# Performance work log

Hardware: AMD Instinct MI355X
Metric: run time of the kernel (lower is better)

## Reference

```python
import jax, jax.numpy as jnp
import numpy as np

N, E, D, H = 40000, 640000, 128, 8
DH = D // H  # out_feats per head
EPS = 1e-5


def _layernorm(x, g, b):
    mu = jnp.mean(x, axis=-1, keepdims=True)
    var = jnp.mean(jnp.square(x - mu), axis=-1, keepdims=True)
    return (x - mu) * jax.lax.rsqrt(var + EPS) * g + b


def setup_inputs() -> dict:
    key = jax.random.key(0)
    ks = jax.random.split(key, 12)
    s = 0.02
    return {
        "feat": jax.random.normal(ks[0], (N, D), dtype=jnp.float32),
        "src": jax.random.randint(ks[1], (E,), 0, N, dtype=jnp.int32),
        "dst": jax.random.randint(ks[2], (E,), 0, N, dtype=jnp.int32),
        "Wq": jax.random.normal(ks[3], (D, D), dtype=jnp.float32) * s,
        "Wk": jax.random.normal(ks[4], (D, D), dtype=jnp.float32) * s,
        "Wv": jax.random.normal(ks[5], (D, D), dtype=jnp.float32) * s,
        "ln1_g": jnp.ones((D,), jnp.float32),
        "ln1_b": jnp.zeros((D,), jnp.float32),
        "ln2_g": jnp.ones((D,), jnp.float32),
        "ln2_b": jnp.zeros((D,), jnp.float32),
        "W1": jax.random.normal(ks[6], (D, 4 * D), dtype=jnp.float32) * s,
        "b1": jnp.zeros((4 * D,), jnp.float32),
        "prelu_w": jnp.full((4 * D,), 0.25, jnp.float32),
        "W2": jax.random.normal(ks[7], (4 * D, D), dtype=jnp.float32) * s,
        "b2": jnp.zeros((D,), jnp.float32),
    }


def reference(feat, src, dst, Wq, Wk, Wv, ln1_g, ln1_b, ln2_g, ln2_b,
              W1, b1, prelu_w, W2, b2):
    n = feat.shape[0]
    feat_c = jax.lax.stop_gradient(feat)  # .clone().detach()
    q = (feat @ Wq).reshape(n, H, DH)
    k = (feat_c @ Wk).reshape(n, H, DH)
    v = (feat_c @ Wv).reshape(n, H, DH)

    # u_dot_v: per-edge, per-head dot product of k at src and q at dst
    scores = jnp.einsum('ehd,ehd->eh', k[src], q[dst]) / np.float32(np.sqrt(DH * H))

    # edge_softmax: softmax over incoming edges of each destination node
    smax = jax.ops.segment_max(scores, dst, num_segments=n)  # [N,H]
    sexp = jnp.exp(scores - smax[dst])
    ssum = jax.ops.segment_sum(sexp, dst, num_segments=n)
    a = sexp / ssum[dst]  # [E,H]  (attn_drop is eval no-op)

    # u_mul_e + sum: weighted scatter-aggregate of v[src] into dst
    msgs = v[src] * a[:, :, None]  # [E,H,DH]
    ft2 = jax.ops.segment_sum(msgs, dst, num_segments=n).reshape(n, D)

    rst = _layernorm(ft2 + feat, ln1_g, ln1_b)
    h = rst @ W1 + b1
    h = jnp.where(h >= 0, h, prelu_w * h)  # PReLU, per-channel
    ffn = h @ W2 + b2  # ffn_drop is eval no-op
    return _layernorm(rst + ffn, ln2_g, ln2_b)
```

## Files before the change

kernel.cpp:

```cpp
#include <hip/hip_runtime.h>
#include <hip/hip_bf16.h>
#include <math.h>

#define DIM 128
#define NHEAD 8
#define DHEAD 16
#define HID 512
#define LN_EPS 1e-5f
#define QSCALE 0.12751879104863297f

typedef __bf16 bf16x8 __attribute__((ext_vector_type(8)));
typedef float f32x4 __attribute__((ext_vector_type(4)));
typedef float f32x2 __attribute__((ext_vector_type(2)));
typedef _Float16 f16x2 __attribute__((ext_vector_type(2)));

__device__ inline float bf2f(unsigned int bits16) {
    return __uint_as_float(bits16 << 16);
}
__device__ inline unsigned short f2bf(float f) {
    unsigned int u = __float_as_uint(f);
    unsigned int r = u + 0x7fff + ((u >> 16) & 1);
    return (unsigned short)(r >> 16);
}
__device__ inline unsigned short f2h(float f) {
    _Float16 h = (_Float16)f;
    return __builtin_bit_cast(unsigned short, h);
}
__device__ inline float h2f(unsigned short h) {
    return (float)__builtin_bit_cast(_Float16, h);
}
__device__ inline unsigned short pk_fp8(float a, float b) {
    int r = __builtin_amdgcn_cvt_pk_fp8_f32(a, b, 0, false);
    return (unsigned short)(r & 0xffff);
}
__device__ inline f32x2 unpk_fp8_lo(unsigned int w) {
    return __builtin_amdgcn_cvt_pk_f32_fp8((int)w, false);
}
__device__ inline f32x2 unpk_fp8_hi(unsigned int w) {
    return __builtin_amdgcn_cvt_pk_f32_fp8((int)w, true);
}
__device__ inline float fexp2(float x) { return __builtin_amdgcn_exp2f(x); }

__device__ inline void gload_lds16(const void* g, void* l) {
    __builtin_amdgcn_global_load_lds(
        (const __attribute__((address_space(1))) unsigned int*)g,
        (__attribute__((address_space(3))) unsigned int*)l, 16, 0, 0);
}

__device__ __forceinline__ float dot16_fp8(uint4 w, const float (&q)[16]) {
    f32x2 a0 = unpk_fp8_lo(w.x), b0 = unpk_fp8_hi(w.x);
    f32x2 a1 = unpk_fp8_lo(w.y), b1 = unpk_fp8_hi(w.y);
    f32x2 a2 = unpk_fp8_lo(w.z), b2 = unpk_fp8_hi(w.z);
    f32x2 a3 = unpk_fp8_lo(w.w), b3 = unpk_fp8_hi(w.w);
    float t0 = fmaf(a0.x, q[0],  fmaf(a0.y, q[1],  fmaf(b0.x, q[2],  b0.y * q[3])));
    float t1 = fmaf(a1.x, q[4],  fmaf(a1.y, q[5],  fmaf(b1.x, q[6],  b1.y * q[7])));
    float t2 = fmaf(a2.x, q[8],  fmaf(a2.y, q[9],  fmaf(b2.x, q[10], b2.y * q[11])));
    float t3 = fmaf(a3.x, q[12], fmaf(a3.y, q[13], fmaf(b3.x, q[14], b3.y * q[15])));
    return (t0 + t1) + (t2 + t3);
}

__device__ __forceinline__ void pv16_fp8(uint4 w, float wt, float (&acc)[16]) {
    f32x2 a0 = unpk_fp8_lo(w.x), b0 = unpk_fp8_hi(w.x);
    f32x2 a1 = unpk_fp8_lo(w.y), b1 = unpk_fp8_hi(w.y);
    f32x2 a2 = unpk_fp8_lo(w.z), b2 = unpk_fp8_hi(w.z);
    f32x2 a3 = unpk_fp8_lo(w.w), b3 = unpk_fp8_hi(w.w);
    acc[0]  = fmaf(a0.x, wt, acc[0]);  acc[1]  = fmaf(a0.y, wt, acc[1]);
    acc[2]  = fmaf(b0.x, wt, acc[2]);  acc[3]  = fmaf(b0.y, wt, acc[3]);
    acc[4]  = fmaf(a1.x, wt, acc[4]);  acc[5]  = fmaf(a1.y, wt, acc[5]);
    acc[6]  = fmaf(b1.x, wt, acc[6]);  acc[7]  = fmaf(b1.y, wt, acc[7]);
    acc[8]  = fmaf(a2.x, wt, acc[8]);  acc[9]  = fmaf(a2.y, wt, acc[9]);
    acc[10] = fmaf(b2.x, wt, acc[10]); acc[11] = fmaf(b2.y, wt, acc[11]);
    acc[12] = fmaf(a3.x, wt, acc[12]); acc[13] = fmaf(a3.y, wt, acc[13]);
    acc[14] = fmaf(b3.x, wt, acc[14]); acc[15] = fmaf(b3.y, wt, acc[15]);
}

__global__ __launch_bounds__(256) void prep_count_kernel(
        int* counts, int* __restrict__ ranks, int Nn,
        const float* __restrict__ feat, unsigned short* __restrict__ featb,
        const float* __restrict__ Wq, const float* __restrict__ Wk, const float* __restrict__ Wv,
        unsigned short* __restrict__ Wqkvt,
        const float* __restrict__ W1, unsigned short* __restrict__ W1t,
        const float* __restrict__ W2, unsigned short* __restrict__ W2t,
        const int* __restrict__ dst, int E, int fb, int wb) {
    int blk = blockIdx.x, t = threadIdx.x;
    if (blk < fb) {
        int i = blk * 256 + t;
        if (i < Nn * 32) {
            float4 v = *(const float4*)(feat + (size_t)i * 4);
            ushort4 o;
            o.x = f2bf(v.x); o.y = f2bf(v.y); o.z = f2bf(v.z); o.w = f2bf(v.w);
            *(ushort4*)(featb + (size_t)i * 4) = o;
        }
    } else if (blk < wb) {
        int b2_ = blk - fb;
        if (b2_ < 192) {
            int sec = b2_ >> 6;
            const float* W = sec == 0 ? Wq : (sec == 1 ? Wk : Wv);
            int o = (b2_ & 63) * 256 + t;
            int oc = o >> 7, orow = o & 127;
            Wqkvt[sec * 16384 + o] = f2bf(W[(size_t)orow * 128 + oc]);
        } else if (b2_ < 448) {
            int o = (b2_ - 192) * 256 + t;
            int oc = o >> 7, orow = o & 127;
            W1t[o] = f2bf(W1[(size_t)orow * 512 + oc]);
        } else {
            int o = (b2_ - 448) * 256 + t;
            int oc = o >> 9, orow = o & 511;
            W2t[o] = f2bf(W2[(size_t)orow * 128 + oc]);
        }
    } else {
        int e0 = (blk - wb) * 1024 + t * 4;
        if (e0 + 3 < E) {
            int4 d = *(const int4*)(dst + e0);
            int4 r;
            r.x = atomicAdd(&counts[d.x], 1);
            r.y = atomicAdd(&counts[d.y], 1);
            r.z = atomicAdd(&counts[d.z], 1);
            r.w = atomicAdd(&counts[d.w], 1);
            *(int4*)(ranks + e0) = r;
        } else {
            for (int e = e0; e < E; ++e) ranks[e] = atomicAdd(&counts[dst[e]], 1);
        }
    }
}


__global__ __launch_bounds__(256) void scanA_kernel(const int* __restrict__ counts, int* bsum, int Nn) {
    int blk = blockIdx.x, t = threadIdx.x;
    int i = blk * 1024 + t * 4;
    int s = 0;
    if (i < Nn) { int4 x = *(const int4*)(counts + i); s = x.x + x.y + x.z + x.w; }
#pragma unroll
    for (int off = 1; off < 64; off <<= 1) s += __shfl_xor(s, off, 64);
    __shared__ int wt[4];
    if ((t & 63) == 0) wt[t >> 6] = s;
    __syncthreads();
    if (t == 0) bsum[blk] = wt[0] + wt[1] + wt[2] + wt[3];
}

__global__ __launch_bounds__(256) void scanC_kernel(const int* __restrict__ counts, const int* __restrict__ bsum,
                                                    int* offsets, int Nn, int NCH) {
    int blk = blockIdx.x, t = threadIdx.x, lane = t & 63, wv = t >> 6;
    __shared__ int wt[4];
    __shared__ int base_s;
    if (wv == 0) {
        int v = (lane < NCH) ? bsum[lane] : 0;
        int s = v;
#pragma unroll
        for (int off = 1; off < 64; off <<= 1) {
            int u = __shfl_up(s, off, 64);
            if (lane >= off) s += u;
        }
        int basev = (blk > 0) ? __shfl(s, blk - 1, 64) : 0;
        int tot = __shfl(s, NCH - 1, 64);
        if (lane == 0) {
            base_s = basev;
            if (blk == 0) offsets[Nn] = tot;
        }
    }
    int i = blk * 1024 + t * 4;
    int4 x = make_int4(0, 0, 0, 0);
    if (i < Nn) x = *(const int4*)(counts + i);
    int ts = x.x + x.y + x.z + x.w;
    int s = ts;
#pragma unroll
    for (int off = 1; off < 64; off <<= 1) {
        int u = __shfl_up(s, off, 64);
        if (lane >= off) s += u;
    }
    if (lane == 63) wt[wv] = s;
    __syncthreads();
    int woff = 0;
    for (int wi = 0; wi < wv; ++wi) woff += wt[wi];
    int excl = base_s + woff + (s - ts);
    if (i < Nn) {
        int o0 = excl, o1 = o0 + x.x, o2 = o1 + x.y, o3 = o2 + x.z;
        *(int4*)(offsets + i) = make_int4(o0, o1, o2, o3);
    }
}

#define QST 136
__global__ __launch_bounds__(256) void fill_qkv_kernel(
        const int* __restrict__ dst, const int* __restrict__ src,
        const int* __restrict__ ranks, const int* __restrict__ offsets,
        int* __restrict__ srcs, int E, int cb,
        const unsigned short* __restrict__ A, const unsigned short* __restrict__ Bt,
        unsigned short* __restrict__ qb, unsigned char* __restrict__ kv8) {
    int blk = blockIdx.x, t = threadIdx.x;
    if (blk < cb) {
        int e0 = blk * 1024 + t * 4;
        if (e0 + 3 < E) {
            int4 d = *(const int4*)(dst + e0);
            int4 sv = *(const int4*)(src + e0);
            int4 rk = *(const int4*)(ranks + e0);
            srcs[offsets[d.x] + rk.x] = sv.x;
            srcs[offsets[d.y] + rk.y] = sv.y;
            srcs[offsets[d.z] + rk.z] = sv.z;
            srcs[offsets[d.w] + rk.w] = sv.w;
        } else {
            for (int e = e0; e < E; ++e) srcs[offsets[dst[e]] + ranks[e]] = src[e];
        }
        return;
    }
    __shared__ unsigned short smem[128 * QST];
    unsigned short* As = smem;
    unsigned short* Bs = smem + 4096;
    int q = blk - cb;
    int region = q % 3;
    int m0 = (q / 3) * 128;
    int wave = t >> 6, lane = t & 63;
    int wr = wave >> 1, wc = wave & 1;
    int lrow = lane & 15, kq = lane >> 4;
    int n0 = region * 128;
    int srow = t >> 2, scol8 = (t & 3) * 8;

    f32x4 acc[4][4] = {};
    for (int k0 = 0; k0 < 128; k0 += 32) {
        gload_lds16(A + (size_t)(m0 + srow) * 128 + k0 + scol8,      As + t * 8);
        gload_lds16(A + (size_t)(m0 + 64 + srow) * 128 + k0 + scol8, As + 2048 + t * 8);
        gload_lds16(Bt + (size_t)(n0 + srow) * 128 + k0 + scol8,      Bs + t * 8);
        gload_lds16(Bt + (size_t)(n0 + 64 + srow) * 128 + k0 + scol8, Bs + 2048 + t * 8);
        __syncthreads();
        bf16x8 af[4], bfr[4];
#pragma unroll
        for (int mi = 0; mi < 4; ++mi)
            af[mi] = *(const bf16x8*)(&As[(wr * 64 + mi * 16 + lrow) * 32 + kq * 8]);
#pragma unroll
        for (int ni = 0; ni < 4; ++ni)
            bfr[ni] = *(const bf16x8*)(&Bs[(wc * 64 + ni * 16 + lrow) * 32 + kq * 8]);
#pragma unroll
        for (int mi = 0; mi < 4; ++mi)
#pragma unroll
            for (int ni = 0; ni < 4; ++ni)
                acc[mi][ni] = __builtin_amdgcn_mfma_f32_16x16x32_bf16(af[mi], bfr[ni], acc[mi][ni], 0, 0, 0);
        __syncthreads();
    }

    float scale = (region == 0) ? QSCALE : 1.f;
#pragma unroll
    for (int ni = 0; ni < 4; ++ni) {
        int col = wc * 64 + ni * 16 + lrow;
#pragma unroll
        for (int mi = 0; mi < 4; ++mi) {
#pragma unroll
            for (int r = 0; r < 4; ++r) {
                int row = wr * 64 + mi * 16 + kq * 4 + r;
                smem[row * QST + col] = f2h(acc[mi][ni][r] * scale);
            }
        }
    }
    __syncthreads();
    if (region == 0) {
        unsigned short* outp = qb + (size_t)m0 * 128;
#pragma unroll
        for (int i = 0; i < 8; ++i) {
            int chunk = i * 256 + t;
            int row = chunk >> 4, c16 = chunk & 15;
            *(float4*)(outp + (size_t)chunk * 8) = *(const float4*)(smem + row * QST + c16 * 8);
        }
    } else {
        int half = region - 1;
#pragma unroll
        for (int i = 0; i < 4; ++i) {
            int chunk = i * 256 + t;
            int row = chunk >> 3, seg = chunk & 7;
            const unsigned short* sp = smem + row * QST + seg * 16;
            unsigned int ow[4];
#pragma unroll
            for (int j = 0; j < 4; ++j) {
                unsigned int lo = pk_fp8(h2f(sp[4 * j]), h2f(sp[4 * j + 1]));
                unsigned int hi = pk_fp8(h2f(sp[4 * j + 2]), h2f(sp[4 * j + 3]));
                ow[j] = lo | (hi << 16);
            }
            *(uint4*)(kv8 + (size_t)(m0 + row) * 256 + half * 128 + seg * 16) =
                make_uint4(ow[0], ow[1], ow[2], ow[3]);
        }
    }
}

__global__ __launch_bounds__(256) void agg_ln1_kernel(
        const unsigned short* __restrict__ qb, const unsigned char* __restrict__ kv8,
        const float* __restrict__ feat,
        const int* __restrict__ srcs, const int* __restrict__ offsets,
        const float* __restrict__ g, const float* __restrict__ b,
        unsigned short* __restrict__ rstb, int n) {
    int node = blockIdx.x * 4 + (threadIdx.x >> 6);
    int lane = threadIdx.x & 63;
    if (node >= n) return;
    int el = lane >> 3;
    int h  = lane & 7;

    const uint4* qp = (const uint4*)(qb + (size_t)node * 128 + h * 16);
    uint4 qlo = qp[0], qhi = qp[1];
    float qf[16];
    {
        unsigned int qw[8] = {qlo.x, qlo.y, qlo.z, qlo.w, qhi.x, qhi.y, qhi.z, qhi.w};
#pragma unroll
        for (int j = 0; j < 8; ++j) {
            f16x2 p2 = __builtin_bit_cast(f16x2, qw[j]);
            qf[2 * j]     = (float)p2.x;
            qf[2 * j + 1] = (float)p2.y;
        }
    }

    int beg = offsets[node], end = offsets[node + 1];
    float l = 0.f;
    float acc[16];
#pragma unroll
    for (int j = 0; j < 16; ++j) acc[j] = 0.f;

    for (int idx = beg; idx < end; idx += 16) {
        int e0i = idx + el, e1i = idx + 8 + el;
        bool v0 = e0i < end, v1 = e1i < end;
        int s0 = srcs[v0 ? e0i : beg];
        int s1 = srcs[v1 ? e1i : beg];
        const uint4* kp0 = (const uint4*)(kv8 + (size_t)s0 * 256 + h * 16);
        const uint4* kp1 = (const uint4*)(kv8 + (size_t)s1 * 256 + h * 16);
        uint4 kw0 = kp0[0];
        uint4 vw0 = kp0[8];
        uint4 kw1 = kp1[0];
        uint4 vw1 = kp1[8];

        float p0 = dot16_fp8(kw0, qf);
        float p1 = dot16_fp8(kw1, qf);
        float sc0 = v0 ? fminf(fmaxf(p0, -30.f), 30.f) : -1000.f;
        float sc1 = v1 ? fminf(fmaxf(p1, -30.f), 30.f) : -1000.f;
        float w0 = fexp2(sc0);
        float w1 = fexp2(sc1);
        l += w0 + w1;
        pv16_fp8(vw0, w0, acc);
        pv16_fp8(vw1, w1, acc);
    }

    l += __shfl_xor(l, 8, 64);
    l += __shfl_xor(l, 16, 64);
    l += __shfl_xor(l, 32, 64);

    float r8[8];
    {
        bool b0 = (el & 1) != 0;
#pragma unroll
        for (int j = 0; j < 8; ++j) {
            float send = b0 ? acc[j] : acc[j + 8];
            float keep = b0 ? acc[j + 8] : acc[j];
            r8[j] = keep + __shfl_xor(send, 8, 64);
        }
    }
    float r4[4];
    {
        bool b1 = (el & 2) != 0;
#pragma unroll
        for (int j = 0; j < 4; ++j) {
            float send = b1 ? r8[j] : r8[j + 4];
            float keep = b1 ? r8[j + 4] : r8[j];
            r4[j] = keep + __shfl_xor(send, 16, 64);
        }
    }
    float r2[2];
    {
        bool b2 = (el & 4) != 0;
#pragma unroll
        for (int j = 0; j < 2; ++j) {
            float send = b2 ? r4[j] : r4[j + 2];
            float keep = b2 ? r4[j + 2] : r4[j];
            r2[j] = keep + __shfl_xor(send, 32, 64);
        }
    }
    int off = ((el & 1) << 3) | ((el & 2) << 1) | ((el & 4) >> 1);
    int d0 = h * 16 + off;

    float inv = (l > 0.f) ? 1.f / l : 0.f;
    float2 fv = *(const float2*)(feat + (size_t)node * DIM + d0);
    float x0 = r2[0] * inv + fv.x;
    float x1 = r2[1] * inv + fv.y;

    float s1 = x0 + x1;
    float s2 = x0 * x0 + x1 * x1;
#pragma unroll
    for (int off2 = 1; off2 < 64; off2 <<= 1) {
        s1 += __shfl_xor(s1, off2, 64);
        s2 += __shfl_xor(s2, off2, 64);
    }
    float mean = s1 * (1.f / DIM);
    float var = s2 * (1.f / DIM) - mean * mean;
    float rinv = rsqrtf(var + LN_EPS);
    float2 gv = *(const float2*)(g + d0);
    float2 bv = *(const float2*)(b + d0);
    float o0 = (x0 - mean) * rinv * gv.x + bv.x;
    float o1 = (x1 - mean) * rinv * gv.y + bv.y;
    unsigned int packed = (unsigned int)f2bf(o0) | ((unsigned int)f2bf(o1) << 16);
    ((unsigned int*)rstb)[(size_t)node * 64 + (d0 >> 1)] = packed;
}

__global__ __launch_bounds__(256) void ffn1_gemm(
        const unsigned short* __restrict__ A, const unsigned short* __restrict__ Bt,
        unsigned short* __restrict__ hid,
        const float* __restrict__ b1, const float* __restrict__ prelu) {
    __shared__ unsigned short smem[128 * QST];
    unsigned short* As = smem;
    unsigned short* Bs = smem + 4096;
    int t = threadIdx.x;
    int wave = t >> 6, lane = t & 63;
    int wr = wave >> 1, wc = wave & 1;
    int lrow = lane & 15, kq = lane >> 4;
    int m0 = blockIdx.y * 128;
    int n0 = blockIdx.x * 128;
    int srow = t >> 2, scol8 = (t & 3) * 8;

    f32x4 acc[4][4] = {};
    for (int k0 = 0; k0 < 128; k0 += 32) {
        gload_lds16(A + (size_t)(m0 + srow) * 128 + k0 + scol8,      As + t * 8);
        gload_lds16(A + (size_t)(m0 + 64 + srow) * 128 + k0 + scol8, As + 2048 + t * 8);
        gload_lds16(Bt + (size_t)(n0 + srow) * 128 + k0 + scol8,      Bs + t * 8);
        gload_lds16(Bt + (size_t)(n0 + 64 + srow) * 128 + k0 + scol8, Bs + 2048 + t * 8);
        __syncthreads();
        bf16x8 af[4], bfr[4];
#pragma unroll
        for (int mi = 0; mi < 4; ++mi)
            af[mi] = *(const bf16x8*)(&As[(wr * 64 + mi * 16 + lrow) * 32 + kq * 8]);
#pragma unroll
        for (int ni = 0; ni < 4; ++ni)
            bfr[ni] = *(const bf16x8*)(&Bs[(wc * 64 + ni * 16 + lrow) * 32 + kq * 8]);
#pragma unroll
        for (int mi = 0; mi < 4; ++mi)
#pragma unroll
            for (int ni = 0; ni < 4; ++ni)
                acc[mi][ni] = __builtin_amdgcn_mfma_f32_16x16x32_bf16(af[mi], bfr[ni], acc[mi][ni], 0, 0, 0);
        __syncthreads();
    }

#pragma unroll
    for (int ni = 0; ni < 4; ++ni) {
        int col = wc * 64 + ni * 16 + lrow;
        int cg = n0 + col;
        float biv = b1[cg], pwv = prelu[cg];
#pragma unroll
        for (int mi = 0; mi < 4; ++mi) {
#pragma unroll
            for (int r = 0; r < 4; ++r) {
                int row = wr * 64 + mi * 16 + kq * 4 + r;
                float v = acc[mi][ni][r] + biv;
                v = v >= 0.f ? v : pwv * v;
                smem[row * QST + col] = f2bf(v);
            }
        }
    }
    __syncthreads();
#pragma unroll
    for (int i = 0; i < 8; ++i) {
        int chunk = i * 256 + t;
        int row = chunk >> 4, c16 = chunk & 15;
        *(float4*)(hid + (size_t)(m0 + row) * 512 + n0 + c16 * 8) =
            *(const float4*)(smem + row * QST + c16 * 8);
    }
}

__global__ __launch_bounds__(256) void ffn2_ln2_kernel(
        const unsigned short* __restrict__ hid, const unsigned short* __restrict__ W2t,
        const unsigned short* __restrict__ rstb,
        const float* __restrict__ b2, const float* __restrict__ g, const float* __restrict__ bb,
        float* __restrict__ out, int Nn) {
    __shared__ unsigned short As[64 * 32];
    __shared__ unsigned short Bs[128 * 32];
    __shared__ float redS[64][4];
    __shared__ float redQ[64][4];
    int t = threadIdx.x;
    int wave = t >> 6, lane = t & 63;
    int lrow = lane & 15, kq = lane >> 4;
    int m0 = blockIdx.x * 64;
    int srow = t >> 2, scol8 = (t & 3) * 8;

    f32x4 acc[4][2] = {};
    for (int k0 = 0; k0 < 512; k0 += 32) {
        gload_lds16(hid + (size_t)(m0 + srow) * 512 + k0 + scol8, As + t * 8);
        gload_lds16(W2t + (size_t)srow * 512 + k0 + scol8,        Bs + t * 8);
        gload_lds16(W2t + (size_t)(64 + srow) * 512 + k0 + scol8, Bs + 2048 + t * 8);
        __syncthreads();
        bf16x8 af[4], bfr[2];
#pragma unroll
        for (int mi = 0; mi < 4; ++mi)
            af[mi] = *(const bf16x8*)(&As[(mi * 16 + lrow) * 32 + kq * 8]);
#pragma unroll
        for (int ni = 0; ni < 2; ++ni)
            bfr[ni] = *(const bf16x8*)(&Bs[(wave * 32 + ni * 16 + lrow) * 32 + kq * 8]);
#pragma unroll
        for (int mi = 0; mi < 4; ++mi)
#pragma unroll
            for (int ni = 0; ni < 2; ++ni)
                acc[mi][ni] = __builtin_amdgcn_mfma_f32_16x16x32_bf16(af[mi], bfr[ni], acc[mi][ni], 0, 0, 0);
        __syncthreads();
    }

    float b2v[2], gv[2], bv[2];
    int cols[2];
#pragma unroll
    for (int ni = 0; ni < 2; ++ni) {
        cols[ni] = wave * 32 + ni * 16 + lrow;
        b2v[ni] = b2[cols[ni]]; gv[ni] = g[cols[ni]]; bv[ni] = bb[cols[ni]];
    }
#pragma unroll
    for (int mi = 0; mi < 4; ++mi) {
#pragma unroll
        for (int r = 0; r < 4; ++r) {
            int rloc = mi * 16 + kq * 4 + r;
            int row = m0 + rloc;
            float ps = 0.f, pq = 0.f;
#pragma unroll
            for (int ni = 0; ni < 2; ++ni) {
                float rsv = bf2f(rstb[(size_t)row * 128 + cols[ni]]);
                float v = acc[mi][ni][r] + b2v[ni] + rsv;
                acc[mi][ni][r] = v;
                ps += v; pq += v * v;
            }
#pragma unroll
            for (int off = 1; off < 16; off <<= 1) {
                ps += __shfl_xor(ps, off, 16);
                pq += __shfl_xor(pq, off, 16);
            }
            if (lrow == 0) { redS[rloc][wave] = ps; redQ[rloc][wave] = pq; }
        }
    }
    __syncthreads();
#pragma unroll
    for (int mi = 0; mi < 4; ++mi) {
#pragma unroll
        for (int r = 0; r < 4; ++r) {
            int rloc = mi * 16 + kq * 4 + r;
            int row = m0 + rloc;
            float s1 = redS[rloc][0] + redS[rloc][1] + redS[rloc][2] + redS[rloc][3];
            float sq = redQ[rloc][0] + redQ[rloc][1] + redQ[rloc][2] + redQ[rloc][3];
            float mean = s1 * (1.f / DIM);
            float var = sq * (1.f / DIM) - mean * mean;
            float rs = rsqrtf(var + LN_EPS);
            if (row < Nn) {
#pragma unroll
                for (int ni = 0; ni < 2; ++ni)
                    out[(size_t)row * 128 + cols[ni]] =
                        (acc[mi][ni][r] - mean) * rs * gv[ni] + bv[ni];
            }
        }
    }
}


extern "C" void kernel_launch(void* const* d_in, const int* in_sizes, int n_in,
                              void* d_out, int out_size, void* d_ws, size_t ws_size,
                              hipStream_t stream) {
    const float* feat   = (const float*)d_in[0];
    const int*   src    = (const int*)d_in[1];
    const int*   dst    = (const int*)d_in[2];
    const float* Wq     = (const float*)d_in[3];
    const float* Wk     = (const float*)d_in[4];
    const float* Wv     = (const float*)d_in[5];
    const float* ln1_g  = (const float*)d_in[6];
    const float* ln1_b  = (const float*)d_in[7];
    const float* ln2_g  = (const float*)d_in[8];
    const float* ln2_b  = (const float*)d_in[9];
    const float* W1     = (const float*)d_in[10];
    const float* b1     = (const float*)d_in[11];
    const float* prelu  = (const float*)d_in[12];
    const float* W2     = (const float*)d_in[13];
    const float* b2     = (const float*)d_in[14];
    float* out = (float*)d_out;

    const int Nn = in_sizes[0] / DIM;
    const int E  = in_sizes[1];
    const int MP = (Nn + 127) & ~127;

    char* w = (char*)d_ws;
    unsigned short* qb   = (unsigned short*)w; w += (size_t)MP * DIM * 2;
    unsigned char*  kv8  = (unsigned char*)w;  w += (size_t)MP * 256;
    unsigned short* rstb = (unsigned short*)w; w += (size_t)MP * DIM * 2;
    unsigned short* featb= (unsigned short*)w; w += (size_t)MP * DIM * 2;
    unsigned short* hid  = (unsigned short*)w; w += (size_t)MP * HID * 2;
    unsigned short* Wqkvt= (unsigned short*)w; w += 3 * DIM * DIM * 2;
    unsigned short* W1t  = (unsigned short*)w; w += (size_t)HID * DIM * 2;
    unsigned short* W2t  = (unsigned short*)w; w += (size_t)DIM * HID * 2;
    int* counts  = (int*)w;  w += (size_t)Nn * 4;
    int* offsets = (int*)w;  w += (size_t)(Nn + 4) * 4;
    int* bsum    = (int*)w;  w += 64 * 4;
    int* srcs    = (int*)w;
    int* ranks   = (int*)hid;

    const int NCH = (Nn + 1023) / 1024;
    const int FB  = Nn / 8;
    const int WB  = FB + 704;
    const int CB  = (E + 1023) / 1024;

    hipMemsetAsync(counts, 0, (size_t)Nn * 4, stream);

    prep_count_kernel<<<WB + CB, 256, 0, stream>>>(
        counts, ranks, Nn, feat, featb, Wq, Wk, Wv, Wqkvt, W1, W1t, W2, W2t, dst, E, FB, WB);

    scanA_kernel<<<NCH, 256, 0, stream>>>(counts, bsum, Nn);
    scanC_kernel<<<NCH, 256, 0, stream>>>(counts, bsum, offsets, Nn, NCH);

    fill_qkv_kernel<<<CB + 3 * (MP / 128), 256, 0, stream>>>(
        dst, src, ranks, offsets, srcs, E, CB, featb, Wqkvt, qb, kv8);

    agg_ln1_kernel<<<(Nn + 3) / 4, 256, 0, stream>>>(qb, kv8, feat,
                                                     srcs, offsets, ln1_g, ln1_b, rstb, Nn);

    {
        dim3 grid(4, MP / 128);
        ffn1_gemm<<<grid, 256, 0, stream>>>(rstb, W1t, hid, b1, prelu);
    }

    ffn2_ln2_kernel<<<MP / 64, 256, 0, stream>>>(hid, W2t, rstb, b2, ln2_g, ln2_b, out, Nn);
}
```

Measured before the change: 234.1 us.

## Fuse FFN1 and FFN2+LN2 into one kernel keeping hidden activations in LDS

```diff
diff --git a/kernel.cpp b/kernel.cpp
--- a/kernel.cpp
+++ b/kernel.cpp
@@ -392,75 +392,13 @@
     ((unsigned int*)rstb)[(size_t)node * 64 + (d0 >> 1)] = packed;
 }
 
-__global__ __launch_bounds__(256) void ffn1_gemm(
-        const unsigned short* __restrict__ A, const unsigned short* __restrict__ Bt,
-        unsigned short* __restrict__ hid,
-        const float* __restrict__ b1, const float* __restrict__ prelu) {
-    __shared__ unsigned short smem[128 * QST];
-    unsigned short* As = smem;
-    unsigned short* Bs = smem + 4096;
-    int t = threadIdx.x;
-    int wave = t >> 6, lane = t & 63;
-    int wr = wave >> 1, wc = wave & 1;
-    int lrow = lane & 15, kq = lane >> 4;
-    int m0 = blockIdx.y * 128;
-    int n0 = blockIdx.x * 128;
-    int srow = t >> 2, scol8 = (t & 3) * 8;
-
-    f32x4 acc[4][4] = {};
-    for (int k0 = 0; k0 < 128; k0 += 32) {
-        gload_lds16(A + (size_t)(m0 + srow) * 128 + k0 + scol8,      As + t * 8);
-        gload_lds16(A + (size_t)(m0 + 64 + srow) * 128 + k0 + scol8, As + 2048 + t * 8);
-        gload_lds16(Bt + (size_t)(n0 + srow) * 128 + k0 + scol8,      Bs + t * 8);
-        gload_lds16(Bt + (size_t)(n0 + 64 + srow) * 128 + k0 + scol8, Bs + 2048 + t * 8);
-        __syncthreads();
-        bf16x8 af[4], bfr[4];
-#pragma unroll
-        for (int mi = 0; mi < 4; ++mi)
-            af[mi] = *(const bf16x8*)(&As[(wr * 64 + mi * 16 + lrow) * 32 + kq * 8]);
-#pragma unroll
-        for (int ni = 0; ni < 4; ++ni)
-            bfr[ni] = *(const bf16x8*)(&Bs[(wc * 64 + ni * 16 + lrow) * 32 + kq * 8]);
-#pragma unroll
-        for (int mi = 0; mi < 4; ++mi)
-#pragma unroll
-            for (int ni = 0; ni < 4; ++ni)
-                acc[mi][ni] = __builtin_amdgcn_mfma_f32_16x16x32_bf16(af[mi], bfr[ni], acc[mi][ni], 0, 0, 0);
-        __syncthreads();
-    }
-
-#pragma unroll
-    for (int ni = 0; ni < 4; ++ni) {
-        int col = wc * 64 + ni * 16 + lrow;
-        int cg = n0 + col;
-        float biv = b1[cg], pwv = prelu[cg];
-#pragma unroll
-        for (int mi = 0; mi < 4; ++mi) {
-#pragma unroll
-            for (int r = 0; r < 4; ++r) {
-                int row = wr * 64 + mi * 16 + kq * 4 + r;
-                float v = acc[mi][ni][r] + biv;
-                v = v >= 0.f ? v : pwv * v;
-                smem[row * QST + col] = f2bf(v);
-            }
-        }
-    }
-    __syncthreads();
-#pragma unroll
-    for (int i = 0; i < 8; ++i) {
-        int chunk = i * 256 + t;
-        int row = chunk >> 4, c16 = chunk & 15;
-        *(float4*)(hid + (size_t)(m0 + row) * 512 + n0 + c16 * 8) =
-            *(const float4*)(smem + row * QST + c16 * 8);
-    }
-}
-
-__global__ __launch_bounds__(256) void ffn2_ln2_kernel(
-        const unsigned short* __restrict__ hid, const unsigned short* __restrict__ W2t,
+__global__ __launch_bounds__(256) void ffn_fused_kernel(
         const unsigned short* __restrict__ rstb,
+        const unsigned short* __restrict__ W1t, const unsigned short* __restrict__ W2t,
+        const float* __restrict__ b1, const float* __restrict__ prelu,
         const float* __restrict__ b2, const float* __restrict__ g, const float* __restrict__ bb,
         float* __restrict__ out, int Nn) {
-    __shared__ unsigned short As[64 * 32];
+    __shared__ unsigned short hidS[64 * 128];
     __shared__ unsigned short Bs[128 * 32];
     __shared__ float redS[64][4];
     __shared__ float redQ[64][4];
@@ -470,25 +408,67 @@
     int m0 = blockIdx.x * 64;
     int srow = t >> 2, scol8 = (t & 3) * 8;
 
-    f32x4 acc[4][2] = {};
-    for (int k0 = 0; k0 < 512; k0 += 32) {
-        gload_lds16(hid + (size_t)(m0 + srow) * 512 + k0 + scol8, As + t * 8);
-        gload_lds16(W2t + (size_t)srow * 512 + k0 + scol8,        Bs + t * 8);
-        gload_lds16(W2t + (size_t)(64 + srow) * 512 + k0 + scol8, Bs + 2048 + t * 8);
+    f32x4 acc2[4][2] = {};
+    for (int n0 = 0; n0 < 4; ++n0) {
+        f32x4 acc1[4][2] = {};
+        for (int kb = 0; kb < 4; ++kb) {
+            gload_lds16(W1t + (size_t)(n0 * 128 + srow) * 128 + kb * 32 + scol8,      Bs + t * 8);
+            gload_lds16(W1t + (size_t)(n0 * 128 + 64 + srow) * 128 + kb * 32 + scol8, Bs + 2048 + t * 8);
+            bf16x8 af[4];
+#pragma unroll
+            for (int mi = 0; mi < 4; ++mi)
+                af[mi] = *(const bf16x8*)(rstb + (size_t)(m0 + mi * 16 + lrow) * 128 + kb * 32 + kq * 8);
+            __syncthreads();
+            bf16x8 bfr[2];
+#pragma unroll
+            for (int ni = 0; ni < 2; ++ni)
+                bfr[ni] = *(const bf16x8*)(&Bs[(wave * 32 + ni * 16 + lrow) * 32 + kq * 8]);
+#pragma unroll
+            for (int mi = 0; mi < 4; ++mi)
+#pragma unroll
+                for (int ni = 0; ni < 2; ++ni)
+                    acc1[mi][ni] = __builtin_amdgcn_mfma_f32_16x16x32_bf16(af[mi], bfr[ni], acc1[mi][ni], 0, 0, 0);
+            __syncthreads();
+        }
+#pragma unroll
+        for (int ni = 0; ni < 2; ++ni) {
+            int col = wave * 32 + ni * 16 + lrow;
+            int cg = n0 * 128 + col;
+            float biv = b1[cg], pwv = prelu[cg];
+#pragma unroll
+            for (int mi = 0; mi < 4; ++mi) {
+#pragma unroll
+                for (int r = 0; r < 4; ++r) {
+                    int row = mi * 16 + kq * 4 + r;
+                    float v = acc1[mi][ni][r] + biv;
+                    v = v >= 0.f ? v : pwv * v;
+                    int blk = (col >> 3) ^ (row & 7);
+                    hidS[row * 128 + blk * 8 + (col & 7)] = f2bf(v);
+                }
+            }
+        }
         __syncthreads();
-        bf16x8 af[4], bfr[2];
-#pragma unroll
-        for (int mi = 0; mi < 4; ++mi)
-            af[mi] = *(const bf16x8*)(&As[(mi * 16 + lrow) * 32 + kq * 8]);
-#pragma unroll
-        for (int ni = 0; ni < 2; ++ni)
-            bfr[ni] = *(const bf16x8*)(&Bs[(wave * 32 + ni * 16 + lrow) * 32 + kq * 8]);
-#pragma unroll
-        for (int mi = 0; mi < 4; ++mi)
+        for (int kb = 0; kb < 4; ++kb) {
+            gload_lds16(W2t + (size_t)srow * 512 + n0 * 128 + kb * 32 + scol8,        Bs + t * 8);
+            gload_lds16(W2t + (size_t)(64 + srow) * 512 + n0 * 128 + kb * 32 + scol8, Bs + 2048 + t * 8);
+            __syncthreads();
+            bf16x8 af[4], bfr[2];
+#pragma unroll
+            for (int mi = 0; mi < 4; ++mi) {
+                int row = mi * 16 + lrow;
+                int blk = (kb * 4 + kq) ^ (row & 7);
+                af[mi] = *(const bf16x8*)(&hidS[row * 128 + blk * 8]);
+            }
 #pragma unroll
             for (int ni = 0; ni < 2; ++ni)
-                acc[mi][ni] = __builtin_amdgcn_mfma_f32_16x16x32_bf16(af[mi], bfr[ni], acc[mi][ni], 0, 0, 0);
-        __syncthreads();
+                bfr[ni] = *(const bf16x8*)(&Bs[(wave * 32 + ni * 16 + lrow) * 32 + kq * 8]);
+#pragma unroll
+            for (int mi = 0; mi < 4; ++mi)
+#pragma unroll
+                for (int ni = 0; ni < 2; ++ni)
+                    acc2[mi][ni] = __builtin_amdgcn_mfma_f32_16x16x32_bf16(af[mi], bfr[ni], acc2[mi][ni], 0, 0, 0);
+            __syncthreads();
+        }
     }
 
     float b2v[2], gv[2], bv[2];
@@ -508,8 +488,8 @@
 #pragma unroll
             for (int ni = 0; ni < 2; ++ni) {
                 float rsv = bf2f(rstb[(size_t)row * 128 + cols[ni]]);
-                float v = acc[mi][ni][r] + b2v[ni] + rsv;
-                acc[mi][ni][r] = v;
+                float v = acc2[mi][ni][r] + b2v[ni] + rsv;
+                acc2[mi][ni][r] = v;
                 ps += v; pq += v * v;
             }
 #pragma unroll
@@ -536,7 +516,7 @@
 #pragma unroll
                 for (int ni = 0; ni < 2; ++ni)
                     out[(size_t)row * 128 + cols[ni]] =
-                        (acc[mi][ni][r] - mean) * rs * gv[ni] + bv[ni];
+                        (acc2[mi][ni][r] - mean) * rs * gv[ni] + bv[ni];
             }
         }
     }
@@ -601,10 +581,6 @@
     agg_ln1_kernel<<<(Nn + 3) / 4, 256, 0, stream>>>(qb, kv8, feat,
                                                      srcs, offsets, ln1_g, ln1_b, rstb, Nn);
 
-    {
-        dim3 grid(4, MP / 128);
-        ffn1_gemm<<<grid, 256, 0, stream>>>(rstb, W1t, hid, b1, prelu);
-    }
-
-    ffn2_ln2_kernel<<<MP / 64, 256, 0, stream>>>(hid, W2t, rstb, b2, ln2_g, ln2_b, out, Nn);
-}
+    ffn_fused_kernel<<<MP / 64, 256, 0, stream>>>(rstb, W1t, W2t, b1, prelu,
+                                                  b2, ln2_g, ln2_b, out, Nn);
+}
```

Result: slower. 245.3 us (+4.8%).

## Load GEMM operands directly into registers and loop over N tiles per block

Applied to the files above, without the earlier changes.

```diff
diff --git a/kernel.cpp b/kernel.cpp
--- a/kernel.cpp
+++ b/kernel.cpp
@@ -40,12 +40,6 @@
     return __builtin_amdgcn_cvt_pk_f32_fp8((int)w, true);
 }
 __device__ inline float fexp2(float x) { return __builtin_amdgcn_exp2f(x); }
-
-__device__ inline void gload_lds16(const void* g, void* l) {
-    __builtin_amdgcn_global_load_lds(
-        (const __attribute__((address_space(1))) unsigned int*)g,
-        (__attribute__((address_space(3))) unsigned int*)l, 16, 0, 0);
-}
 
 __device__ __forceinline__ float dot16_fp8(uint4 w, const float (&q)[16]) {
     f32x2 a0 = unpk_fp8_lo(w.x), b0 = unpk_fp8_hi(w.x);
@@ -202,78 +196,78 @@
         }
         return;
     }
-    __shared__ unsigned short smem[128 * QST];
-    unsigned short* As = smem;
-    unsigned short* Bs = smem + 4096;
-    int q = blk - cb;
-    int region = q % 3;
-    int m0 = (q / 3) * 128;
+    __shared__ unsigned short smem[64 * QST];
+    int m0 = (blk - cb) * 64;
     int wave = t >> 6, lane = t & 63;
-    int wr = wave >> 1, wc = wave & 1;
     int lrow = lane & 15, kq = lane >> 4;
-    int n0 = region * 128;
-    int srow = t >> 2, scol8 = (t & 3) * 8;
-
-    f32x4 acc[4][4] = {};
-    for (int k0 = 0; k0 < 128; k0 += 32) {
-        gload_lds16(A + (size_t)(m0 + srow) * 128 + k0 + scol8,      As + t * 8);
-        gload_lds16(A + (size_t)(m0 + 64 + srow) * 128 + k0 + scol8, As + 2048 + t * 8);
-        gload_lds16(Bt + (size_t)(n0 + srow) * 128 + k0 + scol8,      Bs + t * 8);
-        gload_lds16(Bt + (size_t)(n0 + 64 + srow) * 128 + k0 + scol8, Bs + 2048 + t * 8);
+
+    bf16x8 af[4][4];
+    {
+        const unsigned short* arow = A + (size_t)(m0 + lrow) * 128 + kq * 8;
+#pragma unroll
+        for (int kb = 0; kb < 4; ++kb)
+#pragma unroll
+            for (int mi = 0; mi < 4; ++mi)
+                af[kb][mi] = *(const bf16x8*)(arow + mi * 2048 + kb * 32);
+    }
+
+    for (int region = 0; region < 3; ++region) {
+        const unsigned short* brow =
+            Bt + (size_t)region * 16384 + (size_t)(wave * 32 + lrow) * 128 + kq * 8;
+        f32x4 acc[4][2] = {};
+#pragma unroll
+        for (int kb = 0; kb < 4; ++kb) {
+            bf16x8 bfr[2];
+#pragma unroll
+            for (int ni = 0; ni < 2; ++ni)
+                bfr[ni] = *(const bf16x8*)(brow + ni * 2048 + kb * 32);
+#pragma unroll
+            for (int mi = 0; mi < 4; ++mi)
+#pragma unroll
+                for (int ni = 0; ni < 2; ++ni)
+                    acc[mi][ni] = __builtin_amdgcn_mfma_f32_16x16x32_bf16(af[kb][mi], bfr[ni], acc[mi][ni], 0, 0, 0);
+        }
+
+        float scale = (region == 0) ? QSCALE : 1.f;
+        if (region) __syncthreads();
+#pragma unroll
+        for (int ni = 0; ni < 2; ++ni) {
+            int col = wave * 32 + ni * 16 + lrow;
+#pragma unroll
+            for (int mi = 0; mi < 4; ++mi) {
+#pragma unroll
+                for (int r = 0; r < 4; ++r) {
+                    int row = mi * 16 + kq * 4 + r;
+                    smem[row * QST + col] = f2h(acc[mi][ni][r] * scale);
+                }
+            }
+        }
         __syncthreads();
-        bf16x8 af[4], bfr[4];
-#pragma unroll
-        for (int mi = 0; mi < 4; ++mi)
-            af[mi] = *(const bf16x8*)(&As[(wr * 64 + mi * 16 + lrow) * 32 + kq * 8]);
-#pragma unroll
-        for (int ni = 0; ni < 4; ++ni)
-            bfr[ni] = *(const bf16x8*)(&Bs[(wc * 64 + ni * 16 + lrow) * 32 + kq * 8]);
-#pragma unroll
-        for (int mi = 0; mi < 4; ++mi)
-#pragma unroll
-            for (int ni = 0; ni < 4; ++ni)
-                acc[mi][ni] = __builtin_amdgcn_mfma_f32_16x16x32_bf16(af[mi], bfr[ni], acc[mi][ni], 0, 0, 0);
-        __syncthreads();
-    }
-
-    float scale = (region == 0) ? QSCALE : 1.f;
-#pragma unroll
-    for (int ni = 0; ni < 4; ++ni) {
-        int col = wc * 64 + ni * 16 + lrow;
-#pragma unroll
-        for (int mi = 0; mi < 4; ++mi) {
-#pragma unroll
-            for (int r = 0; r < 4; ++r) {
-                int row = wr * 64 + mi * 16 + kq * 4 + r;
-                smem[row * QST + col] = f2h(acc[mi][ni][r] * scale);
+        if (region == 0) {
+            unsigned short* outp = qb + (size_t)m0 * 128;
+#pragma unroll
+            for (int i = 0; i < 4; ++i) {
+                int chunk = i * 256 + t;
+                int row = chunk >> 4, c16 = chunk & 15;
+                *(float4*)(outp + (size_t)chunk * 8) = *(const float4*)(smem + row * QST + c16 * 8);
             }
-        }
-    }
-    __syncthreads();
-    if (region == 0) {
-        unsigned short* outp = qb + (size_t)m0 * 128;
-#pragma unroll
-        for (int i = 0; i < 8; ++i) {
-            int chunk = i * 256 + t;
-            int row = chunk >> 4, c16 = chunk & 15;
-            *(float4*)(outp + (size_t)chunk * 8) = *(const float4*)(smem + row * QST + c16 * 8);
-        }
-    } else {
-        int half = region - 1;
-#pragma unroll
-        for (int i = 0; i < 4; ++i) {
-            int chunk = i * 256 + t;
-            int row = chunk >> 3, seg = chunk & 7;
-            const unsigned short* sp = smem + row * QST + seg * 16;
-            unsigned int ow[4];
-#pragma unroll
-            for (int j = 0; j < 4; ++j) {
-                unsigned int lo = pk_fp8(h2f(sp[4 * j]), h2f(sp[4 * j + 1]));
-                unsigned int hi = pk_fp8(h2f(sp[4 * j + 2]), h2f(sp[4 * j + 3]));
-                ow[j] = lo | (hi << 16);
+        } else {
+            int half = region - 1;
+#pragma unroll
+            for (int i = 0; i < 2; ++i) {
+                int chunk = i * 256 + t;
+                int row = chunk >> 3, seg = chunk & 7;
+                const unsigned short* sp = smem + row * QST + seg * 16;
+                unsigned int ow[4];
+#pragma unroll
+                for (int j = 0; j < 4; ++j) {
+                    unsigned int lo = pk_fp8(h2f(sp[4 * j]), h2f(sp[4 * j + 1]));
+                    unsigned int hi = pk_fp8(h2f(sp[4 * j + 2]), h2f(sp[4 * j + 3]));
+                    ow[j] = lo | (hi << 16);
+                }
+                *(uint4*)(kv8 + (size_t)(m0 + row) * 256 + half * 128 + seg * 16) =
+                    make_uint4(ow[0], ow[1], ow[2], ow[3]);
             }
-            *(uint4*)(kv8 + (size_t)(m0 + row) * 256 + half * 128 + seg * 16) =
-                make_uint4(ow[0], ow[1], ow[2], ow[3]);
         }
     }
 }
@@ -396,62 +390,64 @@
         const unsigned short* __restrict__ A, const unsigned short* __restrict__ Bt,
         unsigned short* __restrict__ hid,
         const float* __restrict__ b1, const float* __restrict__ prelu) {
-    __shared__ unsigned short smem[128 * QST];
-    unsigned short* As = smem;
-    unsigned short* Bs = smem + 4096;
+    __shared__ unsigned short smem[64 * QST];
     int t = threadIdx.x;
     int wave = t >> 6, lane = t & 63;
-    int wr = wave >> 1, wc = wave & 1;
     int lrow = lane & 15, kq = lane >> 4;
-    int m0 = blockIdx.y * 128;
-    int n0 = blockIdx.x * 128;
-    int srow = t >> 2, scol8 = (t & 3) * 8;
-
-    f32x4 acc[4][4] = {};
-    for (int k0 = 0; k0 < 128; k0 += 32) {
-        gload_lds16(A + (size_t)(m0 + srow) * 128 + k0 + scol8,      As + t * 8);
-        gload_lds16(A + (size_t)(m0 + 64 + srow) * 128 + k0 + scol8, As + 2048 + t * 8);
-        gload_lds16(Bt + (size_t)(n0 + srow) * 128 + k0 + scol8,      Bs + t * 8);
-        gload_lds16(Bt + (size_t)(n0 + 64 + srow) * 128 + k0 + scol8, Bs + 2048 + t * 8);
+    int m0 = blockIdx.x * 64;
+
+    bf16x8 af[4][4];
+    {
+        const unsigned short* arow = A + (size_t)(m0 + lrow) * 128 + kq * 8;
+#pragma unroll
+        for (int kb = 0; kb < 4; ++kb)
+#pragma unroll
+            for (int mi = 0; mi < 4; ++mi)
+                af[kb][mi] = *(const bf16x8*)(arow + mi * 2048 + kb * 32);
+    }
+
+    for (int n0 = 0; n0 < 4; ++n0) {
+        const unsigned short* brow =
+            Bt + (size_t)(n0 * 128 + wave * 32 + lrow) * 128 + kq * 8;
+        f32x4 acc[4][2] = {};
+#pragma unroll
+        for (int kb = 0; kb < 4; ++kb) {
+            bf16x8 bfr[2];
+#pragma unroll
+            for (int ni = 0; ni < 2; ++ni)
+                bfr[ni] = *(const bf16x8*)(brow + ni * 2048 + kb * 32);
+#pragma unroll
+            for (int mi = 0; mi < 4; ++mi)
+#pragma unroll
+                for (int ni = 0; ni < 2; ++ni)
+                    acc[mi][ni] = __builtin_amdgcn_mfma_f32_16x16x32_bf16(af[kb][mi], bfr[ni], acc[mi][ni], 0, 0, 0);
+        }
+
+        if (n0) __syncthreads();
+#pragma unroll
+        for (int ni = 0; ni < 2; ++ni) {
+            int col = wave * 32 + ni * 16 + lrow;
+            int cg = n0 * 128 + col;
+            float biv = b1[cg], pwv = prelu[cg];
+#pragma unroll
+            for (int mi = 0; mi < 4; ++mi) {
+#pragma unroll
+                for (int r = 0; r < 4; ++r) {
+                    int row = mi * 16 + kq * 4 + r;
+                    float v = acc[mi][ni][r] + biv;
+                    v = v >= 0.f ? v : pwv * v;
+                    smem[row * QST + col] = f2bf(v);
+                }
+            }
+        }
         __syncthreads();
-        bf16x8 af[4], bfr[4];
-#pragma unroll
-        for (int mi = 0; mi < 4; ++mi)
-            af[mi] = *(const bf16x8*)(&As[(wr * 64 + mi * 16 + lrow) * 32 + kq * 8]);
-#pragma unroll
-        for (int ni = 0; ni < 4; ++ni)
-            bfr[ni] = *(const bf16x8*)(&Bs[(wc * 64 + ni * 16 + lrow) * 32 + kq * 8]);
-#pragma unroll
-        for (int mi = 0; mi < 4; ++mi)
-#pragma unroll
-            for (int ni = 0; ni < 4; ++ni)
-                acc[mi][ni] = __builtin_amdgcn_mfma_f32_16x16x32_bf16(af[mi], bfr[ni], acc[mi][ni], 0, 0, 0);
-        __syncthreads();
-    }
-
-#pragma unroll
-    for (int ni = 0; ni < 4; ++ni) {
-        int col = wc * 64 + ni * 16 + lrow;
-        int cg = n0 + col;
-        float biv = b1[cg], pwv = prelu[cg];
-#pragma unroll
-        for (int mi = 0; mi < 4; ++mi) {
-#pragma unroll
-            for (int r = 0; r < 4; ++r) {
-                int row = wr * 64 + mi * 16 + kq * 4 + r;
-                float v = acc[mi][ni][r] + biv;
-                v = v >= 0.f ? v : pwv * v;
-                smem[row * QST + col] = f2bf(v);
-            }
-        }
-    }
-    __syncthreads();
-#pragma unroll
-    for (int i = 0; i < 8; ++i) {
-        int chunk = i * 256 + t;
-        int row = chunk >> 4, c16 = chunk & 15;
-        *(float4*)(hid + (size_t)(m0 + row) * 512 + n0 + c16 * 8) =
-            *(const float4*)(smem + row * QST + c16 * 8);
+#pragma unroll
+        for (int i = 0; i < 4; ++i) {
+            int chunk = i * 256 + t;
+            int row = chunk >> 4, c16 = chunk & 15;
+            *(float4*)(hid + (size_t)(m0 + row) * 512 + n0 * 128 + c16 * 8) =
+                *(const float4*)(smem + row * QST + c16 * 8);
+        }
     }
 }
 
@@ -460,35 +456,32 @@
         const unsigned short* __restrict__ rstb,
         const float* __restrict__ b2, const float* __restrict__ g, const float* __restrict__ bb,
         float* __restrict__ out, int Nn) {
-    __shared__ unsigned short As[64 * 32];
-    __shared__ unsigned short Bs[128 * 32];
     __shared__ float redS[64][4];
     __shared__ float redQ[64][4];
     int t = threadIdx.x;
     int wave = t >> 6, lane = t & 63;
     int lrow = lane & 15, kq = lane >> 4;
     int m0 = blockIdx.x * 64;
-    int srow = t >> 2, scol8 = (t & 3) * 8;
 
     f32x4 acc[4][2] = {};
-    for (int k0 = 0; k0 < 512; k0 += 32) {
-        gload_lds16(hid + (size_t)(m0 + srow) * 512 + k0 + scol8, As + t * 8);
-        gload_lds16(W2t + (size_t)srow * 512 + k0 + scol8,        Bs + t * 8);
-        gload_lds16(W2t + (size_t)(64 + srow) * 512 + k0 + scol8, Bs + 2048 + t * 8);
-        __syncthreads();
-        bf16x8 af[4], bfr[2];
-#pragma unroll
-        for (int mi = 0; mi < 4; ++mi)
-            af[mi] = *(const bf16x8*)(&As[(mi * 16 + lrow) * 32 + kq * 8]);
-#pragma unroll
-        for (int ni = 0; ni < 2; ++ni)
-            bfr[ni] = *(const bf16x8*)(&Bs[(wave * 32 + ni * 16 + lrow) * 32 + kq * 8]);
-#pragma unroll
-        for (int mi = 0; mi < 4; ++mi)
+    {
+        const unsigned short* ar = hid + (size_t)(m0 + lrow) * 512 + kq * 8;
+        const unsigned short* br = W2t + (size_t)(wave * 32 + lrow) * 512 + kq * 8;
+#pragma unroll
+        for (int kb = 0; kb < 16; ++kb) {
+            bf16x8 af[4], bfr[2];
+#pragma unroll
+            for (int mi = 0; mi < 4; ++mi)
+                af[mi] = *(const bf16x8*)(ar + mi * 8192 + kb * 32);
 #pragma unroll
             for (int ni = 0; ni < 2; ++ni)
-                acc[mi][ni] = __builtin_amdgcn_mfma_f32_16x16x32_bf16(af[mi], bfr[ni], acc[mi][ni], 0, 0, 0);
-        __syncthreads();
+                bfr[ni] = *(const bf16x8*)(br + ni * 8192 + kb * 32);
+#pragma unroll
+            for (int mi = 0; mi < 4; ++mi)
+#pragma unroll
+                for (int ni = 0; ni < 2; ++ni)
+                    acc[mi][ni] = __builtin_amdgcn_mfma_f32_16x16x32_bf16(af[mi], bfr[ni], acc[mi][ni], 0, 0, 0);
+        }
     }
 
     float b2v[2], gv[2], bv[2];
@@ -588,6 +581,10 @@
     const int CB  = (E + 1023) / 1024;
 
     hipMemsetAsync(counts, 0, (size_t)Nn * 4, stream);
+    if (MP > Nn) {
+        hipMemsetAsync(featb + (size_t)Nn * DIM, 0, (size_t)(MP - Nn) * DIM * 2, stream);
+        hipMemsetAsync(rstb + (size_t)Nn * DIM, 0, (size_t)(MP - Nn) * DIM * 2, stream);
+    }
 
     prep_count_kernel<<<WB + CB, 256, 0, stream>>>(
         counts, ranks, Nn, feat, featb, Wq, Wk, Wv, Wqkvt, W1, W1t, W2, W2t, dst, E, FB, WB);
@@ -595,16 +592,13 @@
     scanA_kernel<<<NCH, 256, 0, stream>>>(counts, bsum, Nn);
     scanC_kernel<<<NCH, 256, 0, stream>>>(counts, bsum, offsets, Nn, NCH);
 
-    fill_qkv_kernel<<<CB + 3 * (MP / 128), 256, 0, stream>>>(
+    fill_qkv_kernel<<<CB + MP / 64, 256, 0, stream>>>(
         dst, src, ranks, offsets, srcs, E, CB, featb, Wqkvt, qb, kv8);
 
     agg_ln1_kernel<<<(Nn + 3) / 4, 256, 0, stream>>>(qb, kv8, feat,
                                                      srcs, offsets, ln1_g, ln1_b, rstb, Nn);
 
-    {
-        dim3 grid(4, MP / 128);
-        ffn1_gemm<<<grid, 256, 0, stream>>>(rstb, W1t, hid, b1, prelu);
-    }
+    ffn1_gemm<<<MP / 64, 256, 0, stream>>>(rstb, W1t, hid, b1, prelu);
 
     ffn2_ln2_kernel<<<MP / 64, 256, 0, stream>>>(hid, W2t, rstb, b2, ln2_g, ln2_b, out, Nn);
 }
```

Measured after the change: 279.5 us. 1.19x slower.
